# Kernel optimization log

Hardware: AMD Instinct MI355X
Metric: run time of the kernel (lower is better)

Reference implementation:

```python
import jax, jax.numpy as jnp
import numpy as np

N_NODES = 100000
N_EDGES = 1600000
D_IN = 13      # per-localization feature dim
D_POS = 3
HIDDEN = 64
D_OUT = 64


def setup_inputs() -> dict:
    key = jax.random.key(0)
    ks = jax.random.split(key, 6)
    x_locs = jax.random.normal(ks[0], (N_NODES, D_IN), dtype=jnp.float32)
    pos_locs = jax.random.uniform(ks[1], (N_NODES, D_POS), dtype=jnp.float32)
    edge_index = jax.random.randint(ks[2], (2, N_EDGES), 0, N_NODES, dtype=jnp.int64)
    fan1 = D_IN + D_POS
    W1 = jax.random.normal(ks[3], (fan1, HIDDEN), dtype=jnp.float32) / np.sqrt(fan1)
    b1 = jnp.zeros((HIDDEN,), dtype=jnp.float32)
    W2 = jax.random.normal(ks[4], (HIDDEN, D_OUT), dtype=jnp.float32) / np.sqrt(HIDDEN)
    b2 = jnp.zeros((D_OUT,), dtype=jnp.float32)
    return {"x_locs": x_locs, "pos_locs": pos_locs, "W1": W1, "b1": b1,
            "W2": W2, "b2": b2, "edge_index": edge_index}


def reference(x_locs, pos_locs, W1, b1, W2, b2, edge_index):
    # PointNetConv (source_to_target): j = edge_index[0] (source), i = edge_index[1] (target)
    src = edge_index[0]
    dst = edge_index[1]
    # message input: [x_j, pos_j - pos_i]  -> [E, D_IN + D_POS]
    msg_in = jnp.concatenate([x_locs[src], pos_locs[src] - pos_locs[dst]], axis=-1)
    # local_nn: Linear -> ReLU -> Linear
    h = jax.nn.relu(msg_in @ W1 + b1)            # [E, HIDDEN]
    h = h @ W2 + b2                               # [E, D_OUT]
    # max aggregation per target node; empty segments get -inf
    agg = jax.ops.segment_max(h, dst, num_segments=N_NODES)  # [N, D_OUT]
    # final .relu() in LocEncoder; also maps empty (-inf) segments to 0 (PyG convention)
    return jax.nn.relu(agg)
```

## Files before the change

kernel.cpp:

```cpp
#include <hip/hip_runtime.h>
#include <hip/hip_bf16.h>


#define N_NODES 100000
#define N_EDGES 1600000
#define NB2  782
#define NBLK 391
#define BATCH 4096
#define SCAP 2400

typedef short short8  __attribute__((ext_vector_type(8)));
typedef float float4v __attribute__((ext_vector_type(4)));

__device__ inline short f2bf(float f) {
    union { float f; unsigned u; } v; v.f = f;
    unsigned u = v.u;
    u += 0x7fffu + ((u >> 16) & 1u);
    return (short)(u >> 16);
}
__device__ inline short2 f2bf2(float a, float b) {
    __hip_bfloat162 h = __float22bfloat162_rn(make_float2(a, b));
    return *(short2*)&h;
}
__device__ inline float bf2f(short s) {
    union { unsigned u; float f; } v;
    v.u = ((unsigned)(unsigned short)s) << 16;
    return v.f;
}
__device__ inline int wave_incl_scan(int v, int lane) {
#pragma unroll
    for (int d = 1; d < 64; d <<= 1) {
        const int t = __shfl_up(v, d);
        if (lane >= d) v += t;
    }
    return v;
}

__global__ __launch_bounds__(256) void prep_kernel(
    const float* __restrict__ x, const float* __restrict__ pos,
    const float* __restrict__ W1, const float* __restrict__ b1,
    const int* __restrict__ ei,
    int* __restrict__ offs,
    int* __restrict__ blockSorted,
    unsigned short* __restrict__ u16, unsigned short* __restrict__ w16)
{
    __shared__ int hist[NB2], eoff[NB2], offc[NB2];
    __shared__ int csumP[13];

    const int tid  = threadIdx.x;
    const int lane = tid & 63;
    const int wv   = tid >> 6;

    if (blockIdx.x >= NBLK) {
        float w1c[16];
#pragma unroll
        for (int k = 0; k < 16; ++k) w1c[k] = W1[k * 64 + lane];
        const float b1c = b1[lane];

        const int waveId = (blockIdx.x - NBLK) * 4 + wv;
        const int nwave  = 512 * 4;

        for (int node = waveId; node < N_NODES; node += nwave) {
            float m = 0.f;
            if (lane < 13) m = x[node * 13 + lane];
            else if (lane < 16) m = pos[node * 3 + (lane - 13)];

            float acc = b1c, accw = 0.f;
#pragma unroll
            for (int k = 0; k < 13; ++k)
                acc = fmaf(__shfl(m, k), w1c[k], acc);
#pragma unroll
            for (int k = 13; k < 16; ++k) {
                const float p = __shfl(m, k);
                acc  = fmaf(p, w1c[k], acc);
                accw = fmaf(p, w1c[k], accw);
            }
            u16[node * 64 + lane] = (unsigned short)f2bf(acc);
            w16[node * 64 + lane] = (unsigned short)f2bf(accw);
        }
        return;
    }

    const int blk = blockIdx.x;
    const int e0  = blk * BATCH;
    const int nn  = (N_EDGES - e0) < BATCH ? (N_EDGES - e0) : BATCH;

    for (int i = tid; i < NB2; i += 256) hist[i] = 0;
    __syncthreads();

#pragma unroll
    for (int rep = 0; rep < 4; ++rep) {
        const int base = rep * 1024 + tid * 4;
        if (base < nn) {
            const int4 d4 = *(const int4*)(ei + N_EDGES + e0 + base);
            atomicAdd(&hist[d4.x >> 7], 1);
            atomicAdd(&hist[d4.y >> 7], 1);
            atomicAdd(&hist[d4.z >> 7], 1);
            atomicAdd(&hist[d4.w >> 7], 1);
        }
    }
    __syncthreads();

    for (int c = wv; c < 13; c += 4) {
        const int idx = c * 64 + lane;
        const int val = (idx < NB2) ? hist[idx] : 0;
        const int inc = wave_incl_scan(val, lane);
        if (idx < NB2) eoff[idx] = inc;
        if (lane == 63) csumP[c] = inc;
    }
    __syncthreads();
    if (tid == 0) {
        int a = 0;
#pragma unroll
        for (int c = 0; c < 13; ++c) { const int t = csumP[c]; csumP[c] = a; a += t; }
    }
    __syncthreads();
    for (int c = wv; c < 13; c += 4) {
        const int idx = c * 64 + lane;
        if (idx < NB2) eoff[idx] += csumP[c] - hist[idx];
    }
    __syncthreads();

    int* orow = offs + blk * (NB2 + 1);
    for (int b = tid; b < NB2; b += 256) { orow[b] = eoff[b]; offc[b] = eoff[b]; }
    if (tid == 0) orow[NB2] = nn;
    __syncthreads();

    int* dstp = blockSorted + blk * BATCH;
#pragma unroll
    for (int rep = 0; rep < 4; ++rep) {
        const int base = rep * 1024 + tid * 4;
        if (base < nn) {
            const int4 s4 = *(const int4*)(ei + e0 + base);
            const int4 d4 = *(const int4*)(ei + N_EDGES + e0 + base);
            int p;
            p = atomicAdd(&offc[d4.x >> 7], 1); dstp[p] = (s4.x << 7) | (d4.x & 127);
            p = atomicAdd(&offc[d4.y >> 7], 1); dstp[p] = (s4.y << 7) | (d4.y & 127);
            p = atomicAdd(&offc[d4.z >> 7], 1); dstp[p] = (s4.z << 7) | (d4.z & 127);
            p = atomicAdd(&offc[d4.w >> 7], 1); dstp[p] = (s4.w << 7) | (d4.w & 127);
        }
    }
}

__global__ __launch_bounds__(256, 2) void aggregate_kernel(
    const unsigned short* __restrict__ u16,
    const unsigned short* __restrict__ w16,
    const float* __restrict__ W2,
    const float* __restrict__ b2,
    const int*   __restrict__ offs,
    const int*   __restrict__ blockSorted,
    float*       __restrict__ out)
{
    __shared__ int   accS[128 * 65];
    __shared__ float wls[128 * 68];
    __shared__ int   staged[SCAP];
    __shared__ int   E[NBLK], G[NBLK];
    __shared__ int   csum[8];
    __shared__ int   totT;

    const int tid  = threadIdx.x;
    const int lane = tid & 63;
    const int wv   = tid >> 6;
    const int q = lane >> 4, n = lane & 15;
    const int b = blockIdx.x;
    const int node0  = b * 128;
    const int nvalid = (N_NODES - node0) < 128 ? (N_NODES - node0) : 128;

    short8 w2f[2][4];
#pragma unroll
    for (int s = 0; s < 2; ++s)
#pragma unroll
        for (int t = 0; t < 4; ++t)
#pragma unroll
            for (int j = 0; j < 8; ++j)
                w2f[s][t][j] = f2bf(W2[(s * 32 + q * 8 + j) * 64 + (n + 16 * t)]);
    float b2c[4];
#pragma unroll
    for (int t = 0; t < 4; ++t) b2c[t] = b2[n + 16 * t];

    for (int i = tid; i < 128 * 65; i += 256) accS[i] = 0;
    for (int i = tid; i < 128 * 32; i += 256) {
        const int row = i >> 5, c = i & 31;
        if (row < nvalid) {
            const int wrd = ((const int*)w16)[(node0 + row) * 32 + c];
            wls[row * 68 + 2 * c]     = bf2f((short)(wrd & 0xffff));
            wls[row * 68 + 2 * c + 1] = bf2f((short)(wrd >> 16));
        }
    }

    for (int r = tid; r < NBLK; r += 256) {
        const int lo = offs[r * (NB2 + 1) + b];
        const int hi = offs[r * (NB2 + 1) + b + 1];
        staged[r] = hi - lo;
        G[r] = r * BATCH + lo;
    }
    __syncthreads();
    for (int c = wv; c < 7; c += 4) {
        const int idx = c * 64 + lane;
        const int val = (idx < NBLK) ? staged[idx] : 0;
        const int inc = wave_incl_scan(val, lane);
        if (idx < NBLK) E[idx] = inc;
        if (lane == 63) csum[c] = inc;
    }
    __syncthreads();
    if (tid == 0) {
        int a = 0;
#pragma unroll
        for (int c = 0; c < 7; ++c) { const int t = csum[c]; csum[c] = a; a += t; }
        totT = a;
    }
    __syncthreads();
    for (int c = wv; c < 7; c += 4) {
        const int idx = c * 64 + lane;
        if (idx < NBLK) E[idx] += csum[c] - staged[idx];
    }
    __syncthreads();

    int T = totT; T = T < SCAP ? T : SCAP;

    for (int i = tid; i < T; i += 256) {
        int lo = 0, hi = NBLK - 1;
#pragma unroll
        for (int s = 0; s < 9; ++s) {
            const int mid = (lo + hi + 1) >> 1;
            if (E[mid] <= i) lo = mid; else hi = mid - 1;
        }
        staged[i] = blockSorted[G[lo] + (i - E[lo])];
    }
    __syncthreads();

    const int tiles = (T + 15) >> 4;
    for (int tile = wv; tile < tiles; tile += 4) {
        const int e  = tile * 16 + n;
        const int wd = staged[e];
        const bool ev = (e < T);
        const int src = ev ? (wd >> 7) : 0;
        const int dln = wd & 127;

        const short8 ulo = *(const short8*)(u16 + src * 64 + q * 8);
        const short8 uhi = *(const short8*)(u16 + src * 64 + 32 + q * 8);
        const float* wr = &wls[dln * 68];
        const float4v wl0 = *(const float4v*)(wr + q * 8);
        const float4v wl1 = *(const float4v*)(wr + q * 8 + 4);
        const float4v wh0 = *(const float4v*)(wr + 32 + q * 8);
        const float4v wh1 = *(const float4v*)(wr + 32 + q * 8 + 4);

        union { short8 v; short2 h[4]; } alo, ahi;
#pragma unroll
        for (int j = 0; j < 2; ++j) {
            alo.h[j]     = f2bf2(fmaxf(bf2f(ulo[2*j])     - wl0[2*j],     0.f),
                                 fmaxf(bf2f(ulo[2*j + 1]) - wl0[2*j + 1], 0.f));
            alo.h[2 + j] = f2bf2(fmaxf(bf2f(ulo[4 + 2*j]) - wl1[2*j],     0.f),
                                 fmaxf(bf2f(ulo[5 + 2*j]) - wl1[2*j + 1], 0.f));
            ahi.h[j]     = f2bf2(fmaxf(bf2f(uhi[2*j])     - wh0[2*j],     0.f),
                                 fmaxf(bf2f(uhi[2*j + 1]) - wh0[2*j + 1], 0.f));
            ahi.h[2 + j] = f2bf2(fmaxf(bf2f(uhi[4 + 2*j]) - wh1[2*j],     0.f),
                                 fmaxf(bf2f(uhi[5 + 2*j]) - wh1[2*j + 1], 0.f));
        }

        float4v c2[4];
#pragma unroll
        for (int t = 0; t < 4; ++t) {
            c2[t] = __builtin_amdgcn_mfma_f32_16x16x32_bf16(
                alo.v, w2f[0][t], (float4v){0.f, 0.f, 0.f, 0.f}, 0, 0, 0);
            c2[t] = __builtin_amdgcn_mfma_f32_16x16x32_bf16(
                ahi.v, w2f[1][t], c2[t], 0, 0, 0);
        }

        const int rowbase = tile * 16 + q * 4;
        const int4 dw = *(const int4*)&staged[rowbase];
        const int dr[4] = {dw.x & 127, dw.y & 127, dw.z & 127, dw.w & 127};
#pragma unroll
        for (int r = 0; r < 4; ++r) {
            const bool rv = (rowbase + r) < T;
#pragma unroll
            for (int t = 0; t < 4; ++t) {
                const float v = c2[t][r] + b2c[t];
                if (rv && v > 0.f)
                    atomicMax(&accS[dr[r] * 65 + n + 16 * t], __float_as_int(v));
            }
        }
    }
    __syncthreads();

    for (int i = tid; i < nvalid * 64; i += 256) {
        const int row = i >> 6, col = i & 63;
        out[(node0 + row) * 64 + col] = __int_as_float(accS[row * 65 + col]);
    }
}

extern "C" void kernel_launch(void* const* d_in, const int* in_sizes, int n_in,
                              void* d_out, int out_size, void* d_ws, size_t ws_size,
                              hipStream_t stream) {
    const float* x   = (const float*)d_in[0];
    const float* pos = (const float*)d_in[1];
    const float* W1  = (const float*)d_in[2];
    const float* b1  = (const float*)d_in[3];
    const float* W2  = (const float*)d_in[4];
    const float* b2  = (const float*)d_in[5];
    const int*   ei  = (const int*)d_in[6];

    char* ws = (char*)d_ws;
    int* blockSorted = (int*)(ws + 0);
    int* offs        = (int*)(ws + 6406144);
    unsigned short* u16 = (unsigned short*)(ws + 7631360);
    unsigned short* w16 = (unsigned short*)(ws + 20431360);

    prep_kernel<<<NBLK + 512, 256, 0, stream>>>(
        x, pos, W1, b1, ei, offs, blockSorted, u16, w16);
    aggregate_kernel<<<NB2, 256, 0, stream>>>(
        u16, w16, W2, b2, offs, blockSorted, (float*)d_out);
}
```

Measured before the change: 218.6 us.

## Transpose offsets, drop LDS w-table, prefetch next tile to raise occupancy

Stores the per-block bucket offsets transposed so the aggregate kernel's reads of each column are contiguous. Removes the 34KB shared-memory fp32 copy of the destination-side W rows and reads the bf16 values straight from global (L2-resident) memory instead, which cuts LDS use enough to allow three blocks per CU. Adds software prefetching of the next tile's gathered operands to overlap load latency with the MFMA and atomic work. The cost is more global traffic per edge and extra register pressure from the double-buffered operands under a tighter launch bound.

```diff
diff --git a/kernel.cpp b/kernel.cpp
--- a/kernel.cpp
+++ b/kernel.cpp
@@ -40,7 +40,7 @@
     const float* __restrict__ x, const float* __restrict__ pos,
     const float* __restrict__ W1, const float* __restrict__ b1,
     const int* __restrict__ ei,
-    int* __restrict__ offs,
+    int* __restrict__ offsT,
     int* __restrict__ blockSorted,
     unsigned short* __restrict__ u16, unsigned short* __restrict__ w16)
 {
@@ -121,9 +121,11 @@
     }
     __syncthreads();
 
-    int* orow = offs + blk * (NB2 + 1);
-    for (int b = tid; b < NB2; b += 256) { orow[b] = eoff[b]; offc[b] = eoff[b]; }
-    if (tid == 0) orow[NB2] = nn;
+    for (int b = tid; b < NB2; b += 256) {
+        offsT[b * NBLK + blk] = eoff[b];
+        offc[b] = eoff[b];
+    }
+    if (tid == 0) offsT[NB2 * NBLK + blk] = nn;
     __syncthreads();
 
     int* dstp = blockSorted + blk * BATCH;
@@ -142,21 +144,20 @@
     }
 }
 
-__global__ __launch_bounds__(256, 2) void aggregate_kernel(
+__global__ __launch_bounds__(256, 3) void aggregate_kernel(
     const unsigned short* __restrict__ u16,
     const unsigned short* __restrict__ w16,
     const float* __restrict__ W2,
     const float* __restrict__ b2,
-    const int*   __restrict__ offs,
+    const int*   __restrict__ offsT,
     const int*   __restrict__ blockSorted,
     float*       __restrict__ out)
 {
-    __shared__ int   accS[128 * 65];
-    __shared__ float wls[128 * 68];
-    __shared__ int   staged[SCAP];
-    __shared__ int   E[NBLK], G[NBLK];
-    __shared__ int   csum[8];
-    __shared__ int   totT;
+    __shared__ int accS[128 * 65];
+    __shared__ int staged[SCAP + 16];
+    __shared__ int E[NBLK], G[NBLK];
+    __shared__ int csum[8];
+    __shared__ int totT;
 
     const int tid  = threadIdx.x;
     const int lane = tid & 63;
@@ -179,18 +180,10 @@
     for (int t = 0; t < 4; ++t) b2c[t] = b2[n + 16 * t];
 
     for (int i = tid; i < 128 * 65; i += 256) accS[i] = 0;
-    for (int i = tid; i < 128 * 32; i += 256) {
-        const int row = i >> 5, c = i & 31;
-        if (row < nvalid) {
-            const int wrd = ((const int*)w16)[(node0 + row) * 32 + c];
-            wls[row * 68 + 2 * c]     = bf2f((short)(wrd & 0xffff));
-            wls[row * 68 + 2 * c + 1] = bf2f((short)(wrd >> 16));
-        }
-    }
 
     for (int r = tid; r < NBLK; r += 256) {
-        const int lo = offs[r * (NB2 + 1) + b];
-        const int hi = offs[r * (NB2 + 1) + b + 1];
+        const int lo = offsT[b * NBLK + r];
+        const int hi = offsT[(b + 1) * NBLK + r];
         staged[r] = hi - lo;
         G[r] = r * BATCH + lo;
     }
@@ -227,35 +220,40 @@
         }
         staged[i] = blockSorted[G[lo] + (i - E[lo])];
     }
+    for (int i = T + tid; i < T + 16; i += 256) staged[i] = 0;
     __syncthreads();
 
     const int tiles = (T + 15) >> 4;
-    for (int tile = wv; tile < tiles; tile += 4) {
+
+    auto load_tile = [&](int tile, int& wd, short8& ulo, short8& uhi,
+                         short8& wl, short8& wh) {
         const int e  = tile * 16 + n;
-        const int wd = staged[e];
+        wd = staged[e];
         const bool ev = (e < T);
         const int src = ev ? (wd >> 7) : 0;
-        const int dln = wd & 127;
-
-        const short8 ulo = *(const short8*)(u16 + src * 64 + q * 8);
-        const short8 uhi = *(const short8*)(u16 + src * 64 + 32 + q * 8);
-        const float* wr = &wls[dln * 68];
-        const float4v wl0 = *(const float4v*)(wr + q * 8);
-        const float4v wl1 = *(const float4v*)(wr + q * 8 + 4);
-        const float4v wh0 = *(const float4v*)(wr + 32 + q * 8);
-        const float4v wh1 = *(const float4v*)(wr + 32 + q * 8 + 4);
+        const int dln = ev ? (wd & 127) : 0;
+        ulo = *(const short8*)(u16 + src * 64 + q * 8);
+        uhi = *(const short8*)(u16 + src * 64 + 32 + q * 8);
+        wl  = *(const short8*)(w16 + (node0 + dln) * 64 + q * 8);
+        wh  = *(const short8*)(w16 + (node0 + dln) * 64 + 32 + q * 8);
+    };
+
+    int tile = wv;
+    int wd; short8 ulo, uhi, wl, wh;
+    if (tile < tiles) load_tile(tile, wd, ulo, uhi, wl, wh);
+
+    for (; tile < tiles; ) {
+        const int tile2 = tile + 4;
+        int wd2; short8 ulo2, uhi2, wl2, wh2;
+        if (tile2 < tiles) load_tile(tile2, wd2, ulo2, uhi2, wl2, wh2);
 
         union { short8 v; short2 h[4]; } alo, ahi;
 #pragma unroll
-        for (int j = 0; j < 2; ++j) {
-            alo.h[j]     = f2bf2(fmaxf(bf2f(ulo[2*j])     - wl0[2*j],     0.f),
-                                 fmaxf(bf2f(ulo[2*j + 1]) - wl0[2*j + 1], 0.f));
-            alo.h[2 + j] = f2bf2(fmaxf(bf2f(ulo[4 + 2*j]) - wl1[2*j],     0.f),
-                                 fmaxf(bf2f(ulo[5 + 2*j]) - wl1[2*j + 1], 0.f));
-            ahi.h[j]     = f2bf2(fmaxf(bf2f(uhi[2*j])     - wh0[2*j],     0.f),
-                                 fmaxf(bf2f(uhi[2*j + 1]) - wh0[2*j + 1], 0.f));
-            ahi.h[2 + j] = f2bf2(fmaxf(bf2f(uhi[4 + 2*j]) - wh1[2*j],     0.f),
-                                 fmaxf(bf2f(uhi[5 + 2*j]) - wh1[2*j + 1], 0.f));
+        for (int j = 0; j < 4; ++j) {
+            alo.h[j] = f2bf2(fmaxf(bf2f(ulo[2*j])   - bf2f(wl[2*j]),   0.f),
+                             fmaxf(bf2f(ulo[2*j+1]) - bf2f(wl[2*j+1]), 0.f));
+            ahi.h[j] = f2bf2(fmaxf(bf2f(uhi[2*j])   - bf2f(wh[2*j]),   0.f),
+                             fmaxf(bf2f(uhi[2*j+1]) - bf2f(wh[2*j+1]), 0.f));
         }
 
         float4v c2[4];
@@ -280,6 +278,9 @@
                     atomicMax(&accS[dr[r] * 65 + n + 16 * t], __float_as_int(v));
             }
         }
+
+        tile = tile2;
+        wd = wd2; ulo = ulo2; uhi = uhi2; wl = wl2; wh = wh2;
     }
     __syncthreads();
 
@@ -302,12 +303,12 @@
 
     char* ws = (char*)d_ws;
     int* blockSorted = (int*)(ws + 0);
-    int* offs        = (int*)(ws + 6406144);
+    int* offsT       = (int*)(ws + 6406144);
     unsigned short* u16 = (unsigned short*)(ws + 7631360);
     unsigned short* w16 = (unsigned short*)(ws + 20431360);
 
     prep_kernel<<<NBLK + 512, 256, 0, stream>>>(
-        x, pos, W1, b1, ei, offs, blockSorted, u16, w16);
+        x, pos, W1, b1, ei, offsT, blockSorted, u16, w16);
     aggregate_kernel<<<NB2, 256, 0, stream>>>(
-        u16, w16, W2, b2, offs, blockSorted, (float*)d_out);
-}
+        u16, w16, W2, b2, offsT, blockSorted, (float*)d_out);
+}
```

Result: no change. 218.8 us (+0.1%).
